# Performance work log

Measured on AMD Instinct MI355X. Metric: run time of the kernel, lower is better.

Reference implementation:

```python
import jax, jax.numpy as jnp
import numpy as np

B, D = 16384, 1280      # batch, EfficientNet-b0 feature dim (model._fc.in_features)
C1, C2, C3 = 8, 6, 4    # fanout per tree level: 8 roots, 6 children each, 4 leaves each


def setup_inputs() -> dict:
    key = jax.random.key(0)
    ks = jax.random.split(key, 7)
    sc = 0.02
    x = jax.random.normal(ks[0], (B, D), dtype=jnp.float32)
    # root classifier: self.final = Linear(1280 -> n[0]=8)
    W_final = jax.random.normal(ks[1], (D, C1), dtype=jnp.float32) * sc
    b_final = jnp.zeros((C1,), dtype=jnp.float32)
    # level-1 node linears: Linear(1281 -> 6); split into feature part Wp and upper-scalar column wu
    Wp1 = jax.random.normal(ks[2], (C1, D, C2), dtype=jnp.float32) * sc
    wu1 = jax.random.normal(ks[3], (C1, C2), dtype=jnp.float32) * sc
    b1 = jnp.zeros((C1, C2), dtype=jnp.float32)
    # level-2 node linears: Linear(1281 -> 4)
    Wp2 = jax.random.normal(ks[4], (C1, C2, D, C3), dtype=jnp.float32) * sc
    wu2 = jax.random.normal(ks[5], (C1, C2, C3), dtype=jnp.float32) * sc
    b2 = jnp.zeros((C1, C2, C3), dtype=jnp.float32)
    return {"x": x, "W_final": W_final, "b_final": b_final,
            "Wp1": Wp1, "wu1": wu1, "b1": b1,
            "Wp2": Wp2, "wu2": wu2, "b2": b2}


def reference(x, W_final, b_final, Wp1, wu1, b1, Wp2, wu2, b2):
    # penultimate = x.clone().detach()
    pen = jax.lax.stop_gradient(x)                      # (B, D)
    # root: raw final-linear outputs (NO softmax at root in the torch code)
    u1 = x @ W_final + b_final                          # (B, C1) == upper for level-1 nodes
    # level-1 nodes: line = softmax(Linear([pen, upper_scalar]))
    # Linear([pen, u]) == pen @ Wp + u * wu + b  (batched over all 8 nodes in one GEMM)
    logits1 = jnp.einsum('bd,idc->bic', pen, Wp1) + u1[:, :, None] * wu1[None] + b1[None]
    p1 = jax.nn.softmax(logits1, axis=-1)               # (B, C1, C2)
    u2 = p1 * u1[:, :, None]                            # upper for level-2 nodes
    # level-2 nodes
    logits2 = jnp.einsum('bd,ijdc->bijc', pen, Wp2) + u2[..., None] * wu2[None] + b2[None]
    p2 = jax.nn.softmax(logits2, axis=-1)               # (B, C1, C2, C3)
    u3 = p2 * u2[..., None]                             # upper for leaf nodes
    # output: for each node (sorted by path length, then lexicographic path),
    # the last column of xdict[node] == upper[node]. Row-major reshape matches
    # the sorted key order for single-char labels.
    return jnp.concatenate([u1, u2.reshape(B, C1 * C2), u3.reshape(B, C1 * C2 * C3)], axis=1)
```

## Files before the change

kernel.cpp:

```cpp
#include <hip/hip_runtime.h>
#include <stdint.h>
#include <stddef.h>

#define D_FEAT 1280
#define N_PAD  256
#define N_OUT  248
#define BM     64
#define BK     64
#define K_ITERS 20
#define W_TILE_BYTES (N_PAD * BK * 2)

typedef float f32x4 __attribute__((ext_vector_type(4)));
typedef short s16x8 __attribute__((ext_vector_type(8)));
typedef unsigned int u32x4 __attribute__((ext_vector_type(4)));

__device__ __forceinline__ unsigned short f2bf(float f) {
  union { float f; unsigned int u; } v; v.f = f;
  unsigned int r = (v.u + 0x7fffu + ((v.u >> 16) & 1u)) >> 16;
  return (unsigned short)r;
}

__device__ __forceinline__ unsigned int cvt_pk(float a, float b) {
  unsigned int r;
  asm("v_cvt_pk_bf16_f32 %0, %1, %2" : "=v"(r) : "v"(a), "v"(b));
  return r;
}

__device__ __forceinline__ void gload16(const void* g, void* l) {
  __builtin_amdgcn_global_load_lds(
      (const __attribute__((address_space(1))) void*)g,
      (__attribute__((address_space(3))) void*)l, 16, 0, 0);
}

__global__ __launch_bounds__(256) void pack_w_kernel(
    const float* __restrict__ Wf, const float* __restrict__ Wp1,
    const float* __restrict__ Wp2, unsigned short* __restrict__ out) {
  int idx = blockIdx.x * 256 + threadIdx.x;
  int e = idx & 7;
  int chunk = idx >> 3;
  int s_phys = chunk & 7;
  int n = (chunk >> 3) & 255;
  int kt = chunk >> 11;
  int s_log = s_phys ^ (n & 7);
  int d = kt * BK + s_log * 8 + e;
  float v = 0.0f;
  if (n < 8) {
    v = Wf[d * 8 + n];
  } else if (n < 56) {
    int m = n - 8;
    v = Wp1[((m / 6) * D_FEAT + d) * 6 + (m % 6)];
  } else if (n < 248) {
    int m = n - 56;
    v = Wp2[(((m / 24) * 6 + ((m % 24) >> 2)) * D_FEAT + d) * 4 + (m & 3)];
  }
  out[idx] = f2bf(v);
}

__global__ __launch_bounds__(512, 2) void tree_head_kernel(
    const float* __restrict__ x, const unsigned short* __restrict__ Wb,
    const float* __restrict__ b_final, const float* __restrict__ wu1,
    const float* __restrict__ b1, const float* __restrict__ wu2,
    const float* __restrict__ b2, float* __restrict__ out) {
  __shared__ __align__(16) char smem[122880];
  char* A0 = smem;
  char* A1 = smem + 8192;
  char* A2 = smem + 16384;
  char* B0 = smem + 24576;
  char* B1 = smem + 57344;
  char* B2 = smem + 90112;

  const int tid  = threadIdx.x;
  const int lane = tid & 63;
  const int wave = tid >> 6;
  const int wm   = wave >> 2;
  const int wn   = wave & 3;
  const int l15  = lane & 15;
  const int lh   = lane >> 4;
  const int row0 = blockIdx.x * BM;

  f32x4 acc[2][4];
#pragma unroll
  for (int m = 0; m < 2; ++m)
#pragma unroll
    for (int n = 0; n < 4; ++n)
#pragma unroll
      for (int j = 0; j < 4; ++j) acc[m][n][j] = 0.0f;

  const int arow = tid >> 3;
  const int aslot = tid & 7;
  const char* aptr = (const char*)x + ((size_t)(row0 + arow) * D_FEAT + aslot * 8) * 4;
  const int awoff = arow * 128 + ((aslot ^ (arow & 7)) << 4);
  const char* bsrc = (const char*)Wb + wave * 1024 + lane * 16;
  const int bdst = wave * 1024;

  f32x4 ra[3][2];

#define STAGEB(kt_, dB_) do {                                                 \
    _Pragma("unroll")                                                         \
    for (int j_ = 0; j_ < 4; ++j_)                                            \
      gload16(bsrc + (size_t)(kt_) * W_TILE_BYTES + j_ * 8192,                \
              (dB_) + bdst + j_ * 8192);                                      \
  } while (0)

#define LOADA(kt_, ri_) do {                                                  \
    ra[ri_][0] = *(const f32x4*)(aptr + (kt_) * 256);                         \
    ra[ri_][1] = *(const f32x4*)(aptr + (kt_) * 256 + 16);                    \
  } while (0)

#define WRITEA(ri_, dA_) do {                                                 \
    union { u32x4 u; s16x8 s; } pk_;                                          \
    pk_.u[0] = cvt_pk(ra[ri_][0][0], ra[ri_][0][1]);                          \
    pk_.u[1] = cvt_pk(ra[ri_][0][2], ra[ri_][0][3]);                          \
    pk_.u[2] = cvt_pk(ra[ri_][1][0], ra[ri_][1][1]);                          \
    pk_.u[3] = cvt_pk(ra[ri_][1][2], ra[ri_][1][3]);                          \
    *(s16x8*)((dA_) + awoff) = pk_.s;                                         \
  } while (0)

#define COMPUTE(cA_, cB_) do {                                                \
    s16x8 fr[2][2];                                                           \
    _Pragma("unroll")                                                         \
    for (int m_ = 0; m_ < 2; ++m_) {                                          \
      int rl_ = wm * 32 + m_ * 16 + l15;                                      \
      _Pragma("unroll")                                                       \
      for (int ks_ = 0; ks_ < 2; ++ks_) {                                     \
        int sl_ = ks_ * 4 + lh;                                               \
        fr[m_][ks_] = *(const s16x8*)((cA_) + rl_ * 128 +                     \
                                      ((sl_ ^ (rl_ & 7)) << 4));              \
      }                                                                       \
    }                                                                         \
    _Pragma("unroll")                                                         \
    for (int ks_ = 0; ks_ < 2; ++ks_) {                                       \
      int sl_ = ks_ * 4 + lh;                                                 \
      _Pragma("unroll")                                                       \
      for (int nf_ = 0; nf_ < 4; ++nf_) {                                     \
        int n_ = wn * 64 + nf_ * 16 + l15;                                    \
        s16x8 b_ = *(const s16x8*)((cB_) + n_ * 128 + ((sl_ ^ (n_ & 7)) << 4));\
        acc[0][nf_] = __builtin_amdgcn_mfma_f32_16x16x32_bf16(fr[0][ks_], b_, acc[0][nf_], 0, 0, 0); \
        acc[1][nf_] = __builtin_amdgcn_mfma_f32_16x16x32_bf16(fr[1][ks_], b_, acc[1][nf_], 0, 0, 0); \
      }                                                                       \
    }                                                                         \
  } while (0)

#define ITER(kt_, cA_, cB_, wA_, sB_, rl_, rc_) do {                          \
    asm volatile("s_waitcnt lgkmcnt(0)" ::: "memory");                        \
    __builtin_amdgcn_sched_barrier(0);                                        \
    __builtin_amdgcn_s_barrier();                                             \
    __builtin_amdgcn_sched_barrier(0);                                        \
    STAGEB((kt_) + 2, sB_);                                                   \
    LOADA((kt_) + 2, rl_);                                                    \
    __builtin_amdgcn_sched_barrier(0);                                        \
    asm volatile("s_waitcnt vmcnt(6)" ::: "memory");                          \
    __builtin_amdgcn_sched_barrier(0);                                        \
    WRITEA(rc_, wA_);                                                         \
    COMPUTE(cA_, cB_);                                                        \
  } while (0)

  STAGEB(0, B0);
  LOADA(0, 0);
  STAGEB(1, B1);
  LOADA(1, 1);
  __builtin_amdgcn_sched_barrier(0);
  asm volatile("s_waitcnt vmcnt(6)" ::: "memory");
  __builtin_amdgcn_sched_barrier(0);
  WRITEA(0, A0);

  for (int t = 0; t < 6; ++t) {
    ITER(3 * t + 0, A0, B0, A1, B2, 2, 1);
    ITER(3 * t + 1, A1, B1, A2, B0, 0, 2);
    ITER(3 * t + 2, A2, B2, A0, B1, 1, 0);
  }

  asm volatile("s_waitcnt lgkmcnt(0)" ::: "memory");
  __builtin_amdgcn_sched_barrier(0);
  __builtin_amdgcn_s_barrier();
  __builtin_amdgcn_sched_barrier(0);
  asm volatile("s_waitcnt vmcnt(0)" ::: "memory");
  __builtin_amdgcn_sched_barrier(0);
  WRITEA(1, A1);
  COMPUTE(A0, B0);

  asm volatile("s_waitcnt lgkmcnt(0)" ::: "memory");
  __builtin_amdgcn_sched_barrier(0);
  __builtin_amdgcn_s_barrier();
  __builtin_amdgcn_sched_barrier(0);
  COMPUTE(A1, B1);

  __syncthreads();

  float* Ls = (float*)smem;
#pragma unroll
  for (int m = 0; m < 2; ++m)
#pragma unroll
    for (int nf = 0; nf < 4; ++nf) {
      int col = wn * 64 + nf * 16 + l15;
      if (col < N_OUT) {
        int rbase = wm * 32 + m * 16 + (lh << 2);
#pragma unroll
        for (int i = 0; i < 4; ++i) Ls[col * 65 + rbase + i] = acc[m][nf][i];
      }
    }
  __syncthreads();

  const int p = tid & 7;
  const int r = tid >> 3;
  float* orow = out + (size_t)(row0 + r) * N_OUT;

  float ui = Ls[p * 65 + r] + b_final[p];
  orow[p] = ui;

  float lg[6];
  float mx = -1e30f;
#pragma unroll
  for (int c = 0; c < 6; ++c) {
    lg[c] = Ls[(8 + p * 6 + c) * 65 + r] + ui * wu1[p * 6 + c] + b1[p * 6 + c];
    mx = fmaxf(mx, lg[c]);
  }
  float s = 0.0f;
#pragma unroll
  for (int c = 0; c < 6; ++c) { lg[c] = __expf(lg[c] - mx); s += lg[c]; }
  float sc = ui / s;
  float u2v[6];
#pragma unroll
  for (int c = 0; c < 6; ++c) {
    u2v[c] = lg[c] * sc;
    orow[8 + p * 6 + c] = u2v[c];
  }

#pragma unroll
  for (int j = 0; j < 6; ++j) {
    int g = p * 6 + j;
    float ug = u2v[j];
    float l2[4];
    float m2 = -1e30f;
#pragma unroll
    for (int c = 0; c < 4; ++c) {
      l2[c] = Ls[(56 + g * 4 + c) * 65 + r] + ug * wu2[g * 4 + c] + b2[g * 4 + c];
      m2 = fmaxf(m2, l2[c]);
    }
    float s2 = 0.0f;
#pragma unroll
    for (int c = 0; c < 4; ++c) { l2[c] = __expf(l2[c] - m2); s2 += l2[c]; }
    float sc2 = ug / s2;
    f32x4 o;
#pragma unroll
    for (int c = 0; c < 4; ++c) o[c] = l2[c] * sc2;
    *(f32x4*)(orow + 56 + g * 4) = o;
  }
#undef STAGEB
#undef LOADA
#undef WRITEA
#undef COMPUTE
#undef ITER
}

extern "C" void kernel_launch(void* const* d_in, const int* in_sizes, int n_in,
                              void* d_out, int out_size, void* d_ws, size_t ws_size,
                              hipStream_t stream) {
  const float* x   = (const float*)d_in[0];
  const float* Wf  = (const float*)d_in[1];
  const float* bf  = (const float*)d_in[2];
  const float* Wp1 = (const float*)d_in[3];
  const float* wu1 = (const float*)d_in[4];
  const float* b1  = (const float*)d_in[5];
  const float* Wp2 = (const float*)d_in[6];
  const float* wu2 = (const float*)d_in[7];
  const float* b2  = (const float*)d_in[8];
  float* out = (float*)d_out;
  unsigned short* Wb = (unsigned short*)d_ws;

  pack_w_kernel<<<1280, 256, 0, stream>>>(Wf, Wp1, Wp2, Wb);
  tree_head_kernel<<<16384 / BM, 512, 0, stream>>>(x, Wb, bf, wu1, b1, wu2, b2, out);
}
```

Before: 35.86 us.

## Deepen A-tile register prefetch to three stages and vectorize weight packing

The GEMM main loop now issues global loads for the A (x) tile three K-steps ahead instead of two, using three register slots and waiting with vmcnt(8). The loop tail is restructured to drain the deeper pipeline. Separately, the weight pack kernel has each thread produce eight bf16 values with packed conversion and one 16-byte store, launched with an eighth as many blocks. The deeper prefetch is meant to hide global load latency better, at the cost of more live registers, which could hurt occupancy or cause spills.

```diff
diff --git a/kernel.cpp b/kernel.cpp
--- a/kernel.cpp
+++ b/kernel.cpp
@@ -35,25 +35,33 @@
 __global__ __launch_bounds__(256) void pack_w_kernel(
     const float* __restrict__ Wf, const float* __restrict__ Wp1,
     const float* __restrict__ Wp2, unsigned short* __restrict__ out) {
-  int idx = blockIdx.x * 256 + threadIdx.x;
-  int e = idx & 7;
-  int chunk = idx >> 3;
+  int chunk = blockIdx.x * 256 + threadIdx.x;
   int s_phys = chunk & 7;
   int n = (chunk >> 3) & 255;
   int kt = chunk >> 11;
   int s_log = s_phys ^ (n & 7);
-  int d = kt * BK + s_log * 8 + e;
-  float v = 0.0f;
+  int d0 = kt * BK + s_log * 8;
+  float v[8];
+#pragma unroll
+  for (int e = 0; e < 8; ++e) v[e] = 0.0f;
   if (n < 8) {
-    v = Wf[d * 8 + n];
+#pragma unroll
+    for (int e = 0; e < 8; ++e) v[e] = Wf[(d0 + e) * 8 + n];
   } else if (n < 56) {
     int m = n - 8;
-    v = Wp1[((m / 6) * D_FEAT + d) * 6 + (m % 6)];
+    const float* base = Wp1 + (size_t)(m / 6) * D_FEAT * 6 + (m % 6);
+#pragma unroll
+    for (int e = 0; e < 8; ++e) v[e] = base[(d0 + e) * 6];
   } else if (n < 248) {
     int m = n - 56;
-    v = Wp2[(((m / 24) * 6 + ((m % 24) >> 2)) * D_FEAT + d) * 4 + (m & 3)];
-  }
-  out[idx] = f2bf(v);
+    const float* base = Wp2 + ((size_t)(m / 24) * 6 + ((m % 24) >> 2)) * D_FEAT * 4 + (m & 3);
+#pragma unroll
+    for (int e = 0; e < 8; ++e) v[e] = base[(d0 + e) * 4];
+  }
+  union { u32x4 u; s16x8 s; } pk;
+#pragma unroll
+  for (int h = 0; h < 4; ++h) pk.u[h] = cvt_pk(v[2 * h], v[2 * h + 1]);
+  *(s16x8*)(out + (size_t)chunk * 8) = pk.s;
 }
 
 __global__ __launch_bounds__(512, 2) void tree_head_kernel(
@@ -141,34 +149,48 @@
     }                                                                         \
   } while (0)
 
-#define ITER(kt_, cA_, cB_, wA_, sB_, rl_, rc_) do {                          \
+#define ITER(kt_, cA_, cB_, wA_, sB_, ls_, ws_) do {                          \
     asm volatile("s_waitcnt lgkmcnt(0)" ::: "memory");                        \
     __builtin_amdgcn_sched_barrier(0);                                        \
     __builtin_amdgcn_s_barrier();                                             \
     __builtin_amdgcn_sched_barrier(0);                                        \
     STAGEB((kt_) + 2, sB_);                                                   \
-    LOADA((kt_) + 2, rl_);                                                    \
-    __builtin_amdgcn_sched_barrier(0);                                        \
-    asm volatile("s_waitcnt vmcnt(6)" ::: "memory");                          \
-    __builtin_amdgcn_sched_barrier(0);                                        \
-    WRITEA(rc_, wA_);                                                         \
+    LOADA((kt_) + 3, ls_);                                                    \
+    __builtin_amdgcn_sched_barrier(0);                                        \
+    asm volatile("s_waitcnt vmcnt(8)" ::: "memory");                          \
+    __builtin_amdgcn_sched_barrier(0);                                        \
+    WRITEA(ws_, wA_);                                                         \
     COMPUTE(cA_, cB_);                                                        \
   } while (0)
 
   STAGEB(0, B0);
   LOADA(0, 0);
+  LOADA(1, 1);
   STAGEB(1, B1);
-  LOADA(1, 1);
+  LOADA(2, 2);
+  __builtin_amdgcn_sched_barrier(0);
+  asm volatile("s_waitcnt vmcnt(8)" ::: "memory");
+  __builtin_amdgcn_sched_barrier(0);
+  WRITEA(0, A0);
+
+  for (int t = 0; t < 5; ++t) {
+    ITER(3 * t + 0, A0, B0, A1, B2, 0, 1);
+    ITER(3 * t + 1, A1, B1, A2, B0, 1, 2);
+    ITER(3 * t + 2, A2, B2, A0, B1, 2, 0);
+  }
+  ITER(15, A0, B0, A1, B2, 0, 1);
+  ITER(16, A1, B1, A2, B0, 1, 2);
+
+  asm volatile("s_waitcnt lgkmcnt(0)" ::: "memory");
+  __builtin_amdgcn_sched_barrier(0);
+  __builtin_amdgcn_s_barrier();
+  __builtin_amdgcn_sched_barrier(0);
+  STAGEB(19, B1);
   __builtin_amdgcn_sched_barrier(0);
   asm volatile("s_waitcnt vmcnt(6)" ::: "memory");
   __builtin_amdgcn_sched_barrier(0);
   WRITEA(0, A0);
-
-  for (int t = 0; t < 6; ++t) {
-    ITER(3 * t + 0, A0, B0, A1, B2, 2, 1);
-    ITER(3 * t + 1, A1, B1, A2, B0, 0, 2);
-    ITER(3 * t + 2, A2, B2, A0, B1, 1, 0);
-  }
+  COMPUTE(A2, B2);
 
   asm volatile("s_waitcnt lgkmcnt(0)" ::: "memory");
   __builtin_amdgcn_sched_barrier(0);
@@ -268,6 +290,6 @@
   float* out = (float*)d_out;
   unsigned short* Wb = (unsigned short*)d_ws;
 
-  pack_w_kernel<<<1280, 256, 0, stream>>>(Wf, Wp1, Wp2, Wb);
+  pack_w_kernel<<<160, 256, 0, stream>>>(Wf, Wp1, Wp2, Wb);
   tree_head_kernel<<<16384 / BM, 512, 0, stream>>>(x, Wb, bf, wu1, b1, wu2, b2, out);
 }
```

After: 34.98 us. -2.5%, faster.
